# Performance work log

Measured on AMD Instinct MI355X. Metric: run time of the kernel, lower is better.

The kernel has to match this reference:

```python
import jax, jax.numpy as jnp
import numpy as np

D = 512       # d_model
H = 8         # n_heads per pathway MHA
CTX_H = 2     # router context_attention heads
P = 16        # num_attention_pathways
K = 8         # top_k_pathways
B = 8
S = 1024
TEMP = 1.0
RH1, RH2 = 128, 64  # router hidden sizes


def mha(x, in_w, in_b, out_w, out_b, n_heads):
    """torch.nn.MultiheadAttention (batch_first, eval mode, no mask)."""
    b, s, d = x.shape
    dh = d // n_heads
    qkv = x @ in_w.T + in_b                      # [b,s,3d]
    q, k, v = jnp.split(qkv, 3, axis=-1)
    sh = lambda t: t.reshape(b, s, n_heads, dh).transpose(0, 2, 1, 3)
    q, k, v = sh(q), sh(k), sh(v)
    scale = 1.0 / float(np.sqrt(dh))
    attn = jax.nn.softmax(jnp.einsum('bhqd,bhkd->bhqk', q, k) * scale, axis=-1)
    o = jnp.einsum('bhqk,bhkd->bhqd', attn, v).transpose(0, 2, 1, 3).reshape(b, s, d)
    return o @ out_w.T + out_b


def setup_inputs() -> dict:
    key = jax.random.key(0)
    ks = jax.random.split(key, 16)
    w = 0.05  # weight init scale to keep attention logits sane
    return {
        'x': jax.random.normal(ks[0], (B, S, D), jnp.float32),
        'ctx_in_w': jax.random.normal(ks[1], (3 * D, D), jnp.float32) * w,
        'ctx_in_b': jnp.zeros((3 * D,), jnp.float32),
        'ctx_out_w': jax.random.normal(ks[2], (D, D), jnp.float32) * w,
        'ctx_out_b': jnp.zeros((D,), jnp.float32),
        'r_w1': jax.random.normal(ks[3], (RH1, D), jnp.float32) * w,
        'r_b1': jnp.zeros((RH1,), jnp.float32),
        'r_w2': jax.random.normal(ks[4], (RH2, RH1), jnp.float32) * w,
        'r_b2': jnp.zeros((RH2,), jnp.float32),
        'r_w3': jax.random.normal(ks[5], (P, RH2), jnp.float32) * w,
        'r_b3': jnp.zeros((P,), jnp.float32),
        'p_in_w': jax.random.normal(ks[6], (P, 3 * D, D), jnp.float32) * w,
        'p_in_b': jnp.zeros((P, 3 * D), jnp.float32),
        'p_out_w': jax.random.normal(ks[7], (P, D, D), jnp.float32) * w,
        'p_out_b': jnp.zeros((P, D), jnp.float32),
    }


def reference(x, ctx_in_w, ctx_in_b, ctx_out_w, ctx_out_b,
              r_w1, r_b1, r_w2, r_b2, r_w3, r_b3,
              p_in_w, p_in_b, p_out_w, p_out_b):
    b, s, d = x.shape
    # --- SemanticPathwayRouter ---
    attended = mha(x, ctx_in_w, ctx_in_b, ctx_out_w, ctx_out_b, CTX_H)
    h = jax.nn.relu(attended @ r_w1.T + r_b1)
    h = jax.nn.relu(h @ r_w2.T + r_b2)
    pathway_scores = h @ r_w3.T + r_b3            # [b,s,P]
    # --- GLBL load-balance loss (eval: no buffer updates) ---
    probs_lb = jax.nn.softmax(pathway_scores, axis=-1)
    freq = probs_lb.mean(axis=(0, 1))             # [P] (frequencies == avg scores)
    glbl_loss = P * jnp.sum(freq * freq)
    # --- top-k gating: softmax -> topk scatter -> renormalize ---
    probs = jax.nn.softmax(pathway_scores / TEMP, axis=-1)
    top_v, top_i = jax.lax.top_k(probs, K)        # [b,s,K]
    bi = jnp.arange(b)[:, None, None]
    si = jnp.arange(s)[None, :, None]
    weights = jnp.zeros_like(probs).at[bi, si, top_i].set(top_v)
    weights = weights / (weights.sum(axis=-1, keepdims=True) + 1e-8)
    # --- combine: weighted sum of P full-MHA experts (scan keeps memory low) ---
    wp = jnp.moveaxis(weights, -1, 0)             # [P,b,s]
    def step(acc, params):
        iw, ib, ow, ob, wk = params
        return acc + mha(x, iw, ib, ow, ob, H) * wk[..., None], None
    output, _ = jax.lax.scan(step, jnp.zeros_like(x),
                             (p_in_w, p_in_b, p_out_w, p_out_b, wp))
    return output, glbl_loss, weights
```

## Files before the change

kernel.cpp:

```cpp
#include <hip/hip_runtime.h>
#include <math.h>

#define TOKENS 8192
#define DM 512
#define TD 1536
#define SEQ 1024
#define NPATH 16
#define TOPK 8

typedef __bf16 bf16x8v __attribute__((ext_vector_type(8)));
typedef __bf16 bf16x4v __attribute__((ext_vector_type(4)));
typedef float f32x4v __attribute__((ext_vector_type(4)));
typedef unsigned short u16x8 __attribute__((ext_vector_type(8)));

__device__ __forceinline__ void gload_lds16(const void* gp, unsigned lds_byte_off) {
    __builtin_amdgcn_global_load_lds(
        (const __attribute__((address_space(1))) unsigned int*)(uintptr_t)gp,
        (__attribute__((address_space(3))) unsigned int*)(uintptr_t)lds_byte_off,
        16, 0, 0);
}

__global__ __launch_bounds__(256)
void gemm_f32_nt(const float* __restrict__ A, const float* __restrict__ B,
                 const float* __restrict__ bias, float* __restrict__ C,
                 int M, int N, int K, int lda, int ldb, int ldc,
                 float alpha, int relu, int zmode)
{
    __shared__ float As[16][132];
    __shared__ float Bs[16][132];
    if (zmode == 1) {
        const int z = blockIdx.z, bb = z >> 1, hh = z & 1;
        A += (size_t)bb * SEQ * TD + hh * 256;
        B += (size_t)bb * SEQ * TD + 512 + hh * 256;
        C += (size_t)z * SEQ * SEQ;
    }
    const int tid = threadIdx.x;
    const int bm = blockIdx.y << 7, bn = blockIdx.x << 7;
    const int tx4 = (tid & 15) << 2, ty4 = ((tid >> 4) & 15) << 2;
    float acc[8][8] = {};
    for (int k0 = 0; k0 < K; k0 += 16) {
        __syncthreads();
#pragma unroll
        for (int it = 0; it < 2; ++it) {
            const int u = (it << 8) + tid;
            const int row = u >> 2, kc4 = (u & 3) << 2;
            const float4 av = *(const float4*)(A + (size_t)(bm + row) * lda + k0 + kc4);
            As[kc4 + 0][row] = av.x; As[kc4 + 1][row] = av.y;
            As[kc4 + 2][row] = av.z; As[kc4 + 3][row] = av.w;
            const float4 bv = *(const float4*)(B + (size_t)(bn + row) * ldb + k0 + kc4);
            Bs[kc4 + 0][row] = bv.x; Bs[kc4 + 1][row] = bv.y;
            Bs[kc4 + 2][row] = bv.z; Bs[kc4 + 3][row] = bv.w;
        }
        __syncthreads();
#pragma unroll
        for (int kk = 0; kk < 16; ++kk) {
            const float4 a0 = *(const float4*)&As[kk][ty4];
            const float4 a1 = *(const float4*)&As[kk][64 + ty4];
            const float4 b0 = *(const float4*)&Bs[kk][tx4];
            const float4 b1 = *(const float4*)&Bs[kk][64 + tx4];
            const float aa[8] = {a0.x, a0.y, a0.z, a0.w, a1.x, a1.y, a1.z, a1.w};
            const float bb[8] = {b0.x, b0.y, b0.z, b0.w, b1.x, b1.y, b1.z, b1.w};
#pragma unroll
            for (int i = 0; i < 8; ++i)
#pragma unroll
                for (int j = 0; j < 8; ++j)
                    acc[i][j] = fmaf(aa[i], bb[j], acc[i][j]);
        }
    }
    float bcol[8] = {};
    if (bias) {
        const float4 bL = *(const float4*)(bias + bn + tx4);
        const float4 bH = *(const float4*)(bias + bn + 64 + tx4);
        bcol[0] = bL.x; bcol[1] = bL.y; bcol[2] = bL.z; bcol[3] = bL.w;
        bcol[4] = bH.x; bcol[5] = bH.y; bcol[6] = bH.z; bcol[7] = bH.w;
    }
#pragma unroll
    for (int i = 0; i < 8; ++i) {
        const int row = bm + ((i < 4) ? (ty4 + i) : (64 + ty4 + i - 4));
        float* cp = C + (size_t)row * ldc + bn;
        float v[8];
#pragma unroll
        for (int j = 0; j < 8; ++j) {
            v[j] = alpha * acc[i][j] + bcol[j];
            if (relu) v[j] = fmaxf(v[j], 0.f);
        }
        *(float4*)(cp + tx4) = make_float4(v[0], v[1], v[2], v[3]);
        *(float4*)(cp + 64 + tx4) = make_float4(v[4], v[5], v[6], v[7]);
    }
}

__global__ __launch_bounds__(256)
void gemm_f32_pv(const float* __restrict__ Sb, const float* __restrict__ qkv,
                 float* __restrict__ obuf)
{
    __shared__ float As[16][132];
    __shared__ float Bs[16][128];
    const int z = blockIdx.z, bb = z >> 1, hh = z & 1;
    const float* A = Sb + (size_t)z * SEQ * SEQ;
    const float* B = qkv + (size_t)bb * SEQ * TD + 1024 + hh * 256;
    float* C = obuf + (size_t)bb * SEQ * 512 + hh * 256;
    const int tid = threadIdx.x;
    const int bm = blockIdx.y << 7, bn = blockIdx.x << 7;
    const int tx4 = (tid & 15) << 2, ty4 = ((tid >> 4) & 15) << 2;
    float acc[8][8] = {};
    for (int k0 = 0; k0 < SEQ; k0 += 16) {
        __syncthreads();
#pragma unroll
        for (int it = 0; it < 2; ++it) {
            const int u = (it << 8) + tid;
            const int row = u >> 2, kc4 = (u & 3) << 2;
            const float4 av = *(const float4*)(A + (size_t)(bm + row) * SEQ + k0 + kc4);
            As[kc4 + 0][row] = av.x; As[kc4 + 1][row] = av.y;
            As[kc4 + 2][row] = av.z; As[kc4 + 3][row] = av.w;
            const int krow = u >> 5, n4 = (u & 31) << 2;
            *(float4*)&Bs[krow][n4] = *(const float4*)(B + (size_t)(k0 + krow) * TD + bn + n4);
        }
        __syncthreads();
#pragma unroll
        for (int kk = 0; kk < 16; ++kk) {
            const float4 a0 = *(const float4*)&As[kk][ty4];
            const float4 a1 = *(const float4*)&As[kk][64 + ty4];
            const float4 b0 = *(const float4*)&Bs[kk][tx4];
            const float4 b1 = *(const float4*)&Bs[kk][64 + tx4];
            const float aa[8] = {a0.x, a0.y, a0.z, a0.w, a1.x, a1.y, a1.z, a1.w};
            const float bb[8] = {b0.x, b0.y, b0.z, b0.w, b1.x, b1.y, b1.z, b1.w};
#pragma unroll
            for (int i = 0; i < 8; ++i)
#pragma unroll
                for (int j = 0; j < 8; ++j)
                    acc[i][j] = fmaf(aa[i], bb[j], acc[i][j]);
        }
    }
#pragma unroll
    for (int i = 0; i < 8; ++i) {
        const int row = bm + ((i < 4) ? (ty4 + i) : (64 + ty4 + i - 4));
        float* cp = C + (size_t)row * 512 + bn;
        *(float4*)(cp + tx4) = make_float4(acc[i][0], acc[i][1], acc[i][2], acc[i][3]);
        *(float4*)(cp + 64 + tx4) = make_float4(acc[i][4], acc[i][5], acc[i][6], acc[i][7]);
    }
}

__global__ __launch_bounds__(256)
void softmax_rows(float* __restrict__ S_)
{
    const int row = blockIdx.x * 4 + (threadIdx.x >> 6);
    const int lane = threadIdx.x & 63;
    float* rp = S_ + (size_t)row * 1024 + lane * 16;
    float4 v[4];
#pragma unroll
    for (int i = 0; i < 4; ++i) v[i] = *(const float4*)(rp + i * 4);
    float mx = -INFINITY;
#pragma unroll
    for (int i = 0; i < 4; ++i)
        mx = fmaxf(mx, fmaxf(fmaxf(v[i].x, v[i].y), fmaxf(v[i].z, v[i].w)));
#pragma unroll
    for (int off = 1; off < 64; off <<= 1) mx = fmaxf(mx, __shfl_xor(mx, off));
    float sum = 0.f;
#pragma unroll
    for (int i = 0; i < 4; ++i) {
        v[i].x = __expf(v[i].x - mx); v[i].y = __expf(v[i].y - mx);
        v[i].z = __expf(v[i].z - mx); v[i].w = __expf(v[i].w - mx);
        sum += v[i].x + v[i].y + v[i].z + v[i].w;
    }
#pragma unroll
    for (int off = 1; off < 64; off <<= 1) sum += __shfl_xor(sum, off);
    const float inv = 1.f / sum;
#pragma unroll
    for (int i = 0; i < 4; ++i) {
        v[i].x *= inv; v[i].y *= inv; v[i].z *= inv; v[i].w *= inv;
        *(float4*)(rp + i * 4) = v[i];
    }
}

__global__ __launch_bounds__(256)
void gemm_f32(const float* __restrict__ A, const float* __restrict__ W,
              const float* __restrict__ bias, float* __restrict__ C,
              int M, int N, int K, int relu)
{
    __shared__ float As[16][64];
    __shared__ float Bs[16][64];
    const int bm = blockIdx.y << 6;
    const int bn = blockIdx.x << 6;
    const int tid = threadIdx.x;
    const int tx = tid & 15, ty = tid >> 4;
    const int lr = tid >> 2;
    const int lc = (tid & 3) << 2;
    float acc[4][4] = {};
    for (int k0 = 0; k0 < K; k0 += 16) {
        float4 av = *(const float4*)(A + (size_t)(bm + lr) * K + (k0 + lc));
        float4 bv = make_float4(0.f, 0.f, 0.f, 0.f);
        const int wr = bn + lr;
        if (wr < N) bv = *(const float4*)(W + (size_t)wr * K + (k0 + lc));
        __syncthreads();
        As[lc + 0][lr] = av.x; As[lc + 1][lr] = av.y;
        As[lc + 2][lr] = av.z; As[lc + 3][lr] = av.w;
        Bs[lc + 0][lr] = bv.x; Bs[lc + 1][lr] = bv.y;
        Bs[lc + 2][lr] = bv.z; Bs[lc + 3][lr] = bv.w;
        __syncthreads();
#pragma unroll
        for (int kk = 0; kk < 16; ++kk) {
            const float4 a4 = *(const float4*)(&As[kk][ty << 2]);
            const float4 b4 = *(const float4*)(&Bs[kk][tx << 2]);
            const float a[4] = {a4.x, a4.y, a4.z, a4.w};
            const float b[4] = {b4.x, b4.y, b4.z, b4.w};
#pragma unroll
            for (int i = 0; i < 4; ++i)
#pragma unroll
                for (int j = 0; j < 4; ++j)
                    acc[i][j] = fmaf(a[i], b[j], acc[i][j]);
        }
    }
#pragma unroll
    for (int i = 0; i < 4; ++i) {
        const int m = bm + (ty << 2) + i;
#pragma unroll
        for (int j = 0; j < 4; ++j) {
            const int n = bn + (tx << 2) + j;
            if (n < N) {
                float v = acc[i][j] + bias[n];
                if (relu) v = fmaxf(v, 0.f);
                C[(size_t)m * N + n] = v;
            }
        }
    }
}

template <int DH>
__global__ __launch_bounds__(256)
void flash_attn(const float* __restrict__ qkv, float* __restrict__ O,
                int H, float scale)
{
    constexpr int NU = DH / 64;
    __shared__ float Qs[32][DH + 4];
    __shared__ float Ks[32][DH + 4];
    __shared__ float Vs[32][DH + 4];
    __shared__ float Ps[32][33];
    const int tid = threadIdx.x;
    const int g2 = tid & 15;
    const int rs = tid >> 4;
    const int bh = blockIdx.y;
    const int b = bh / H, h = bh - b * H;
    const int rb = blockIdx.x << 5;
    const float* qb = qkv + (size_t)b * SEQ * TD + (size_t)h * DH;
    const float* kb = qb + DM;
    const float* vb = qb + 2 * DM;

    for (int idx = tid; idx < 32 * (DH / 4); idx += 256) {
        const int rr = idx / (DH / 4);
        const int dp = (idx - rr * (DH / 4)) << 2;
        float4 v = *(const float4*)(qb + (size_t)(rb + rr) * TD + dp);
        v.x *= scale; v.y *= scale; v.z *= scale; v.w *= scale;
        *(float4*)&Qs[rr][dp] = v;
    }
    float m0 = -INFINITY, m1 = -INFINITY, l0 = 0.f, l1 = 0.f;
    float4 o0[NU], o1[NU];
#pragma unroll
    for (int u = 0; u < NU; ++u) {
        o0[u] = make_float4(0.f, 0.f, 0.f, 0.f);
        o1[u] = make_float4(0.f, 0.f, 0.f, 0.f);
    }
    __syncthreads();

    for (int kt = 0; kt < SEQ; kt += 32) {
        for (int idx = tid; idx < 32 * (DH / 4); idx += 256) {
            const int rr = idx / (DH / 4);
            const int dp = (idx - rr * (DH / 4)) << 2;
            *(float4*)&Ks[rr][dp] = *(const float4*)(kb + (size_t)(kt + rr) * TD + dp);
            *(float4*)&Vs[rr][dp] = *(const float4*)(vb + (size_t)(kt + rr) * TD + dp);
        }
        __syncthreads();
        float s00 = 0.f, s01 = 0.f, s10 = 0.f, s11 = 0.f;
        const int cA = g2, cB = g2 + 16;
#pragma unroll 8
        for (int i = 0; i < DH; i += 4) {
            const float4 q0 = *(const float4*)&Qs[rs][i];
            const float4 q1 = *(const float4*)&Qs[rs + 16][i];
            const float4 k0 = *(const float4*)&Ks[cA][i];
            const float4 k1 = *(const float4*)&Ks[cB][i];
            s00 += q0.x * k0.x + q0.y * k0.y + q0.z * k0.z + q0.w * k0.w;
            s01 += q0.x * k1.x + q0.y * k1.y + q0.z * k1.z + q0.w * k1.w;
            s10 += q1.x * k0.x + q1.y * k0.y + q1.z * k0.z + q1.w * k0.w;
            s11 += q1.x * k1.x + q1.y * k1.y + q1.z * k1.z + q1.w * k1.w;
        }
        float ml0 = fmaxf(s00, s01), ml1 = fmaxf(s10, s11);
#pragma unroll
        for (int off = 1; off < 16; off <<= 1) {
            ml0 = fmaxf(ml0, __shfl_xor(ml0, off));
            ml1 = fmaxf(ml1, __shfl_xor(ml1, off));
        }
        const float n0 = fmaxf(m0, ml0), n1 = fmaxf(m1, ml1);
        const float f0 = __expf(m0 - n0), f1 = __expf(m1 - n1);
        const float p00 = __expf(s00 - n0), p01 = __expf(s01 - n0);
        const float p10 = __expf(s10 - n1), p11 = __expf(s11 - n1);
        float sum0 = p00 + p01, sum1 = p10 + p11;
#pragma unroll
        for (int off = 1; off < 16; off <<= 1) {
            sum0 += __shfl_xor(sum0, off);
            sum1 += __shfl_xor(sum1, off);
        }
        l0 = l0 * f0 + sum0; l1 = l1 * f1 + sum1;
        m0 = n0; m1 = n1;
#pragma unroll
        for (int u = 0; u < NU; ++u) {
            o0[u].x *= f0; o0[u].y *= f0; o0[u].z *= f0; o0[u].w *= f0;
            o1[u].x *= f1; o1[u].y *= f1; o1[u].z *= f1; o1[u].w *= f1;
        }
        Ps[rs][cA] = p00; Ps[rs][cB] = p01;
        Ps[rs + 16][cA] = p10; Ps[rs + 16][cB] = p11;
        __syncthreads();
#pragma unroll 4
        for (int c = 0; c < 32; ++c) {
            const float pv0 = Ps[rs][c];
            const float pv1 = Ps[rs + 16][c];
#pragma unroll
            for (int u = 0; u < NU; ++u) {
                const float4 v4 = *(const float4*)&Vs[c][(g2 << 2) + (u << 6)];
                o0[u].x = fmaf(pv0, v4.x, o0[u].x);
                o0[u].y = fmaf(pv0, v4.y, o0[u].y);
                o0[u].z = fmaf(pv0, v4.z, o0[u].z);
                o0[u].w = fmaf(pv0, v4.w, o0[u].w);
                o1[u].x = fmaf(pv1, v4.x, o1[u].x);
                o1[u].y = fmaf(pv1, v4.y, o1[u].y);
                o1[u].z = fmaf(pv1, v4.z, o1[u].z);
                o1[u].w = fmaf(pv1, v4.w, o1[u].w);
            }
        }
        __syncthreads();
    }
    const float i0 = 1.f / l0, i1 = 1.f / l1;
    float* ob0 = O + (size_t)b * SEQ * DM + (size_t)(rb + rs) * DM + h * DH;
    float* ob1 = ob0 + (size_t)16 * DM;
#pragma unroll
    for (int u = 0; u < NU; ++u) {
        float4 w0 = o0[u];
        w0.x *= i0; w0.y *= i0; w0.z *= i0; w0.w *= i0;
        *(float4*)(ob0 + (g2 << 2) + (u << 6)) = w0;
        float4 w1 = o1[u];
        w1.x *= i1; w1.y *= i1; w1.z *= i1; w1.w *= i1;
        *(float4*)(ob1 + (g2 << 2) + (u << 6)) = w1;
    }
}

__global__ __launch_bounds__(256)
void router_epilogue(const float* __restrict__ scores, float* __restrict__ freq,
                     float* __restrict__ weights)
{
    const int t = blockIdx.x * 256 + threadIdx.x;
    float s[NPATH];
#pragma unroll
    for (int i = 0; i < NPATH; ++i) s[i] = scores[(size_t)t * NPATH + i];
    float mx = s[0];
#pragma unroll
    for (int i = 1; i < NPATH; ++i) mx = fmaxf(mx, s[i]);
    float p[NPATH];
    float sum = 0.f;
#pragma unroll
    for (int i = 0; i < NPATH; ++i) { p[i] = expf(s[i] - mx); sum += p[i]; }
    const float inv = 1.f / sum;
#pragma unroll
    for (int i = 0; i < NPATH; ++i) p[i] *= inv;
#pragma unroll
    for (int i = 0; i < NPATH; ++i) {
        float v = p[i];
        for (int off = 32; off >= 1; off >>= 1) v += __shfl_xor(v, off);
        if ((threadIdx.x & 63) == 0) atomicAdd(&freq[i], v);
    }
    unsigned used = 0u;
    float topv[TOPK];
    int topi[TOPK];
    float wsum = 0.f;
#pragma unroll
    for (int k = 0; k < TOPK; ++k) {
        float best = -1.f; int bi = 0;
#pragma unroll
        for (int i = 0; i < NPATH; ++i) {
            if (!((used >> i) & 1u) && p[i] > best) { best = p[i]; bi = i; }
        }
        used |= 1u << bi;
        topv[k] = best; topi[k] = bi;
        wsum += best;
    }
    const float winv = 1.f / (wsum + 1e-8f);
    float w[NPATH];
#pragma unroll
    for (int i = 0; i < NPATH; ++i) w[i] = 0.f;
#pragma unroll
    for (int k = 0; k < TOPK; ++k) w[topi[k]] = topv[k] * winv;
#pragma unroll
    for (int i = 0; i < NPATH; ++i) weights[(size_t)t * NPATH + i] = w[i];
}

__global__ void glbl_loss_kernel(const float* __restrict__ freq, float* __restrict__ out)
{
    if (threadIdx.x == 0 && blockIdx.x == 0) {
        float acc = 0.f;
        for (int i = 0; i < NPATH; ++i) {
            const float f = freq[i] * (1.f / (float)TOKENS);
            acc += f * f;
        }
        out[0] = (float)NPATH * acc;
    }
}

__global__ __launch_bounds__(256)
void cast_f32_bf16(const float* __restrict__ src, __bf16* __restrict__ dst, int n)
{
    const int i = (blockIdx.x * 256 + threadIdx.x) * 4;
    if (i < n) {
        const float4 v = *(const float4*)(src + i);
        bf16x4v o;
        o[0] = (__bf16)v.x; o[1] = (__bf16)v.y; o[2] = (__bf16)v.z; o[3] = (__bf16)v.w;
        *(bf16x4v*)(dst + i) = o;
    }
}

__global__ __launch_bounds__(256)
void gemm_bf16_qkv(const __bf16* __restrict__ A, const __bf16* __restrict__ B,
                   const float* __restrict__ bias, __bf16* __restrict__ C,
                   int N, int K)
{
    __shared__ __attribute__((aligned(16))) __bf16 As[128 * 32];
    __shared__ __attribute__((aligned(16))) __bf16 Bs[128 * 32];
    const int tid = threadIdx.x;
    const int l = tid & 63, w = tid >> 6;
    const int wr = w >> 1, wc = w & 1;
    const int a16 = l & 15, g = l >> 4;
    const int bm = blockIdx.y << 7, bn = blockIdx.x << 7;
    const unsigned asA = (unsigned)(uintptr_t)(void*)&As[0];
    const unsigned asB = (unsigned)(uintptr_t)(void*)&Bs[0];

    f32x4v acc[4][4] = {};
    for (int k0 = 0; k0 < K; k0 += 32) {
        __syncthreads();
#pragma unroll
        for (int it = 0; it < 2; ++it) {
            const int u = it * 256 + tid;
            const int row = u >> 2, cc = u & 3;
            const unsigned dst = (unsigned)((it * 256 + w * 64) * 16);
            gload_lds16(A + (size_t)(bm + row) * K + k0 + cc * 8, asA + dst);
            gload_lds16(B + (size_t)(bn + row) * K + k0 + cc * 8, asB + dst);
        }
        __syncthreads();
        bf16x8v af[4], bf[4];
#pragma unroll
        for (int m = 0; m < 4; ++m)
            af[m] = *(const bf16x8v*)&As[(wr * 64 + m * 16 + a16) * 32 + g * 8];
#pragma unroll
        for (int n = 0; n < 4; ++n)
            bf[n] = *(const bf16x8v*)&Bs[(wc * 64 + n * 16 + a16) * 32 + g * 8];
#pragma unroll
        for (int m = 0; m < 4; ++m)
#pragma unroll
            for (int n = 0; n < 4; ++n)
                acc[m][n] = __builtin_amdgcn_mfma_f32_16x16x32_bf16(af[m], bf[n], acc[m][n], 0, 0, 0);
    }
#pragma unroll
    for (int n = 0; n < 4; ++n) {
        const int col = bn + wc * 64 + n * 16 + a16;
        const float bv = bias[col];
        const float sc = (col < DM) ? 0.125f : 1.0f;
#pragma unroll
        for (int m = 0; m < 4; ++m) {
            const int row0 = bm + wr * 64 + m * 16 + g * 4;
#pragma unroll
            for (int r = 0; r < 4; ++r)
                C[(size_t)(row0 + r) * N + col] = (__bf16)((acc[m][n][r] + bv) * sc);
        }
    }
}

__global__ __launch_bounds__(256)
void gemm_bf16_out(const __bf16* __restrict__ A, const __bf16* __restrict__ B,
                   const float* __restrict__ bias, const float* __restrict__ wts,
                   float* __restrict__ out, int path, int first)
{
    __shared__ __attribute__((aligned(16))) __bf16 As[128 * 32];
    __shared__ __attribute__((aligned(16))) __bf16 Bs[128 * 32];
    const int tid = threadIdx.x;
    const int l = tid & 63, w = tid >> 6;
    const int wr = w >> 1, wc = w & 1;
    const int a16 = l & 15, g = l >> 4;
    const int bm = blockIdx.y << 7, bn = blockIdx.x << 7;
    const unsigned asA = (unsigned)(uintptr_t)(void*)&As[0];
    const unsigned asB = (unsigned)(uintptr_t)(void*)&Bs[0];

    f32x4v acc[4][4] = {};
    for (int k0 = 0; k0 < DM; k0 += 32) {
        __syncthreads();
#pragma unroll
        for (int it = 0; it < 2; ++it) {
            const int u = it * 256 + tid;
            const int row = u >> 2, cc = u & 3;
            const unsigned dst = (unsigned)((it * 256 + w * 64) * 16);
            gload_lds16(A + (size_t)(bm + row) * DM + k0 + cc * 8, asA + dst);
            gload_lds16(B + (size_t)(bn + row) * DM + k0 + cc * 8, asB + dst);
        }
        __syncthreads();
        bf16x8v af[4], bf[4];
#pragma unroll
        for (int m = 0; m < 4; ++m)
            af[m] = *(const bf16x8v*)&As[(wr * 64 + m * 16 + a16) * 32 + g * 8];
#pragma unroll
        for (int n = 0; n < 4; ++n)
            bf[n] = *(const bf16x8v*)&Bs[(wc * 64 + n * 16 + a16) * 32 + g * 8];
#pragma unroll
        for (int m = 0; m < 4; ++m)
#pragma unroll
            for (int n = 0; n < 4; ++n)
                acc[m][n] = __builtin_amdgcn_mfma_f32_16x16x32_bf16(af[m], bf[n], acc[m][n], 0, 0, 0);
    }
#pragma unroll
    for (int m = 0; m < 4; ++m) {
        const int row0 = bm + wr * 64 + m * 16 + g * 4;
#pragma unroll
        for (int r = 0; r < 4; ++r) {
            const int row = row0 + r;
            const float wk = wts[(size_t)row * NPATH + path];
#pragma unroll
            for (int n = 0; n < 4; ++n) {
                const int col = bn + wc * 64 + n * 16 + a16;
                const float v = (acc[m][n][r] + bias[col]) * wk;
                const size_t oi = (size_t)row * DM + col;
                if (first) out[oi] = v; else out[oi] += v;
            }
        }
    }
}

__global__ __launch_bounds__(256)
void attn_bf16(const __bf16* __restrict__ qkv, __bf16* __restrict__ O)
{
    __shared__ __attribute__((aligned(16))) __bf16 Ks[64 * 72];
    __shared__ __attribute__((aligned(16))) __bf16 Vt[64 * 72];
    __shared__ __attribute__((aligned(16))) __bf16 Pq[4][32 * 72];
    const int tid = threadIdx.x;
    const int l = tid & 63, w = tid >> 6;
    const int a = l & 15, g = l >> 4;
    const int bh = blockIdx.y;
    const int b = bh >> 3, h = bh & 7;
    const int qb = blockIdx.x << 7;
    const size_t base = (size_t)b * SEQ * TD;

    bf16x8v qA0, qA1, qB0, qB1;
    {
        const __bf16* qp = qkv + base + (size_t)(qb + w * 32 + a) * TD + h * 64 + g * 8;
        qA0 = *(const bf16x8v*)qp;
        qA1 = *(const bf16x8v*)(qp + 32);
        const __bf16* qp2 = qp + (size_t)16 * TD;
        qB0 = *(const bf16x8v*)qp2;
        qB1 = *(const bf16x8v*)(qp2 + 32);
    }
    float lA = 0.f, lB = 0.f;
    f32x4v oA[4] = {}, oB[4] = {};
    __bf16* pw = &Pq[w][0];
    const int sc8 = tid & 7;
    const int sr  = tid >> 3;
    const int vcol8 = (sr >> 2) ^ sc8;

    bf16x8v kpre0, kpre1, vpre0, vpre1;
    {
        const __bf16* kp0 = qkv + base + (size_t)sr * TD + DM + h * 64 + sc8 * 8;
        kpre0 = *(const bf16x8v*)kp0;
        kpre1 = *(const bf16x8v*)(kp0 + (size_t)32 * TD);
        const __bf16* vp0 = qkv + base + (size_t)(2 * sr) * TD + 2 * DM + h * 64 + sc8 * 8;
        vpre0 = *(const bf16x8v*)vp0;
        vpre1 = *(const bf16x8v*)(vp0 + TD);
    }

    for (int kt = 0; kt < SEQ; kt += 64) {
        __syncthreads();

        *(bf16x8v*)&Ks[sr * 72 + sc8 * 8] = kpre0;
        *(bf16x8v*)&Ks[(32 + sr) * 72 + sc8 * 8] = kpre1;
        {
            const u16x8 v0 = __builtin_bit_cast(u16x8, vpre0);
            const u16x8 v1 = __builtin_bit_cast(u16x8, vpre1);
#pragma unroll
            for (int j = 0; j < 8; ++j) {
                const unsigned pk = (unsigned)v0[j] | ((unsigned)v1[j] << 16);
                *(unsigned*)&Vt[(sc8 * 8 + j) * 72 + vcol8 * 8 + (sr & 3) * 2] = pk;
            }
        }
        if (kt + 64 < SEQ) {
            const __bf16* kp0 = qkv + base + (size_t)(kt + 64 + sr) * TD + DM + h * 64 + sc8 * 8;
            kpre0 = *(const bf16x8v*)kp0;
            kpre1 = *(const bf16x8v*)(kp0 + (size_t)32 * TD);
            const __bf16* vp0 = qkv + base + (size_t)(kt + 64 + 2 * sr) * TD + 2 * DM + h * 64 + sc8 * 8;
            vpre0 = *(const bf16x8v*)vp0;
            vpre1 = *(const bf16x8v*)(vp0 + TD);
        }
        __syncthreads();

        f32x4v sA[4] = {}, sB[4] = {};
        __builtin_amdgcn_s_setprio(1);
#pragma unroll
        for (int kc = 0; kc < 4; ++kc) {
            const bf16x8v kf0 = *(const bf16x8v*)&Ks[(kc * 16 + a) * 72 + g * 8];
            const bf16x8v kf1 = *(const bf16x8v*)&Ks[(kc * 16 + a) * 72 + 32 + g * 8];
            sA[kc] = __builtin_amdgcn_mfma_f32_16x16x32_bf16(kf0, qA0, sA[kc], 0, 0, 0);
            sA[kc] = __builtin_amdgcn_mfma_f32_16x16x32_bf16(kf1, qA1, sA[kc], 0, 0, 0);
            sB[kc] = __builtin_amdgcn_mfma_f32_16x16x32_bf16(kf0, qB0, sB[kc], 0, 0, 0);
            sB[kc] = __builtin_amdgcn_mfma_f32_16x16x32_bf16(kf1, qB1, sB[kc], 0, 0, 0);
        }
        __builtin_amdgcn_s_setprio(0);

        float lsumA = 0.f, lsumB = 0.f;
#pragma unroll
        for (int kc = 0; kc < 4; ++kc) {
            bf16x4v pkA, pkB;
#pragma unroll
            for (int r = 0; r < 4; ++r) {
                const float pA = __expf(sA[kc][r]);
                const float pB = __expf(sB[kc][r]);
                lsumA += pA; lsumB += pB;
                pkA[r] = (__bf16)pA; pkB[r] = (__bf16)pB;
            }
            *(bf16x4v*)&pw[a * 72 + kc * 16 + g * 4] = pkA;
            *(bf16x4v*)&pw[(16 + a) * 72 + kc * 16 + g * 4] = pkB;
        }
        lsumA += __shfl_xor(lsumA, 16);
        lsumA += __shfl_xor(lsumA, 32);
        lsumB += __shfl_xor(lsumB, 16);
        lsumB += __shfl_xor(lsumB, 32);
        lA += lsumA; lB += lsumB;
        asm volatile("s_waitcnt lgkmcnt(0)" ::: "memory");

        __builtin_amdgcn_s_setprio(1);
#pragma unroll
        for (int dc = 0; dc < 4; ++dc) {
            const int vrow = dc * 16 + a;
#pragma unroll
            for (int kh = 0; kh < 2; ++kh) {
                const bf16x8v vf = *(const bf16x8v*)&Vt[vrow * 72 + ((((kh << 2) + g) ^ ((vrow >> 3) & 7)) & 7) * 8];
                const bf16x8v paA = *(const bf16x8v*)&pw[a * 72 + kh * 32 + g * 8];
                const bf16x8v paB = *(const bf16x8v*)&pw[(16 + a) * 72 + kh * 32 + g * 8];
                oA[dc] = __builtin_amdgcn_mfma_f32_16x16x32_bf16(paA, vf, oA[dc], 0, 0, 0);
                oB[dc] = __builtin_amdgcn_mfma_f32_16x16x32_bf16(paB, vf, oB[dc], 0, 0, 0);
            }
        }
        __builtin_amdgcn_s_setprio(0);
    }

    float liA[4], liB[4];
#pragma unroll
    for (int r = 0; r < 4; ++r) {
        liA[r] = 1.f / __shfl(lA, 4 * g + r);
        liB[r] = 1.f / __shfl(lB, 4 * g + r);
    }
    const int row0 = qb + w * 32 + g * 4;
#pragma unroll
    for (int dc = 0; dc < 4; ++dc)
#pragma unroll
        for (int r = 0; r < 4; ++r) {
            O[(size_t)(b * SEQ + row0 + r) * DM + h * 64 + dc * 16 + a] = (__bf16)(oA[dc][r] * liA[r]);
            O[(size_t)(b * SEQ + row0 + 16 + r) * DM + h * 64 + dc * 16 + a] = (__bf16)(oB[dc][r] * liB[r]);
        }
}

extern "C" void kernel_launch(void* const* d_in, const int* in_sizes, int n_in,
                              void* d_out, int out_size, void* d_ws, size_t ws_size,
                              hipStream_t stream)
{
    const float* x         = (const float*)d_in[0];
    const float* ctx_in_w  = (const float*)d_in[1];
    const float* ctx_in_b  = (const float*)d_in[2];
    const float* ctx_out_w = (const float*)d_in[3];
    const float* ctx_out_b = (const float*)d_in[4];
    const float* r_w1      = (const float*)d_in[5];
    const float* r_b1      = (const float*)d_in[6];
    const float* r_w2      = (const float*)d_in[7];
    const float* r_b2      = (const float*)d_in[8];
    const float* r_w3      = (const float*)d_in[9];
    const float* r_b3      = (const float*)d_in[10];
    const float* p_in_w    = (const float*)d_in[11];
    const float* p_in_b    = (const float*)d_in[12];
    const float* p_out_w   = (const float*)d_in[13];
    const float* p_out_b   = (const float*)d_in[14];

    float* out  = (float*)d_out;
    float* loss = out + (size_t)TOKENS * DM;
    float* wts  = loss + 1;

    float* F = (float*)d_ws;
    float* qkvbuf   = F;
    float* obuf     = F + 12582912;
    float* attended = F;
    float* h1       = F + 4194304;
    float* h2       = F + 5242880;
    float* scores   = F + 5767168;
    float* freq     = F + 5898240;

    const int M = TOKENS;
    dim3 blk(256);
    const bool big = ws_size >= (size_t)134217728;

    hipMemsetAsync(freq, 0, NPATH * sizeof(float), stream);
    gemm_f32_nt<<<dim3(TD / 128, M / 128), blk, 0, stream>>>(
        x, ctx_in_w, ctx_in_b, qkvbuf, M, TD, DM, DM, DM, TD, 1.f, 0, 0);
    if (big) {
        float* Sbuf = F + 16777216;
        gemm_f32_nt<<<dim3(8, 8, 16), blk, 0, stream>>>(
            qkvbuf, qkvbuf, nullptr, Sbuf, SEQ, SEQ, 256, TD, TD, SEQ, 0.0625f, 0, 1);
        softmax_rows<<<dim3(16 * SEQ / 4), blk, 0, stream>>>(Sbuf);
        gemm_f32_pv<<<dim3(2, 8, 16), blk, 0, stream>>>(Sbuf, qkvbuf, obuf);
    } else {
        flash_attn<256><<<dim3(SEQ / 32, 8 * 2), blk, 0, stream>>>(qkvbuf, obuf, 2, 1.f / 16.f);
    }
    gemm_f32_nt<<<dim3(DM / 128, M / 128), blk, 0, stream>>>(
        obuf, ctx_out_w, ctx_out_b, attended, M, DM, DM, DM, DM, DM, 1.f, 0, 0);
    gemm_f32_nt<<<dim3(1, M / 128), blk, 0, stream>>>(
        attended, r_w1, r_b1, h1, M, 128, DM, DM, DM, 128, 1.f, 1, 0);
    gemm_f32<<<dim3(1, M / 64), blk, 0, stream>>>(h1, r_w2, r_b2, h2, M, 64, 128, 1);
    gemm_f32<<<dim3(1, M / 64), blk, 0, stream>>>(h2, r_w3, r_b3, scores, M, NPATH, 64, 0);
    router_epilogue<<<dim3(TOKENS / 256), blk, 0, stream>>>(scores, freq, wts);
    glbl_loss_kernel<<<dim3(1), dim3(64), 0, stream>>>(freq, loss);

    if (big) {
        __bf16* xb       = (__bf16*)F;
        __bf16* qkv_b    = (__bf16*)(F + 2097152);
        __bf16* obuf_b   = (__bf16*)(F + 8388608);
        __bf16* wqkv_all = (__bf16*)(F + 16777216);
        __bf16* wout_all = (__bf16*)(F + 23068672);
        cast_f32_bf16<<<dim3(TOKENS * DM / 4 / 256), blk, 0, stream>>>(x, xb, TOKENS * DM);
        cast_f32_bf16<<<dim3(NPATH * TD * DM / 4 / 256), blk, 0, stream>>>(
            p_in_w, wqkv_all, NPATH * TD * DM);
        cast_f32_bf16<<<dim3(NPATH * DM * DM / 4 / 256), blk, 0, stream>>>(
            p_out_w, wout_all, NPATH * DM * DM);
        for (int p = 0; p < NPATH; ++p) {
            gemm_bf16_qkv<<<dim3(TD / 128, M / 128), blk, 0, stream>>>(
                xb, wqkv_all + (size_t)p * TD * DM, p_in_b + (size_t)p * TD, qkv_b, TD, DM);
            attn_bf16<<<dim3(SEQ / 128, 64), blk, 0, stream>>>(qkv_b, obuf_b);
            gemm_bf16_out<<<dim3(DM / 128, M / 128), blk, 0, stream>>>(
                obuf_b, wout_all + (size_t)p * DM * DM, p_out_b + (size_t)p * DM, wts, out, p, p == 0);
        }
    } else {
        __bf16* xb     = (__bf16*)F;
        __bf16* qkv_b  = (__bf16*)(F + 2097152);
        __bf16* obuf_b = (__bf16*)(F + 8388608);
        __bf16* wqkv_b = (__bf16*)(F + 12582912);
        __bf16* wout_b = (__bf16*)(F + 12976128);
        cast_f32_bf16<<<dim3(TOKENS * DM / 4 / 256), blk, 0, stream>>>(x, xb, TOKENS * DM);
        for (int p = 0; p < NPATH; ++p) {
            cast_f32_bf16<<<dim3(TD * DM / 4 / 256), blk, 0, stream>>>(
                p_in_w + (size_t)p * TD * DM, wqkv_b, TD * DM);
            cast_f32_bf16<<<dim3(DM * DM / 4 / 256), blk, 0, stream>>>(
                p_out_w + (size_t)p * DM * DM, wout_b, DM * DM);
            gemm_bf16_qkv<<<dim3(TD / 128, M / 128), blk, 0, stream>>>(
                xb, wqkv_b, p_in_b + (size_t)p * TD, qkv_b, TD, DM);
            attn_bf16<<<dim3(SEQ / 128, 64), blk, 0, stream>>>(qkv_b, obuf_b);
            gemm_bf16_out<<<dim3(DM / 128, M / 128), blk, 0, stream>>>(
                obuf_b, wout_b, p_out_b + (size_t)p * DM, wts, out, p, p == 0);
        }
    }
}
```

Measured before the change: 2.132 ms.

## Split pathway attention across two KV halves with a combine kernel

Replaces the per-pathway attention kernel with a split-K variant that processes each half of the key/value sequence in a separate block. Partial fp32 outputs and row sums go to workspace, and a new combine kernel adds them and normalises into bf16. The goal is to double the attention grid from 512 to 1024 blocks for better occupancy of the GPU's compute units. The cost is an extra kernel launch per pathway plus fp32 partial-output traffic of about 32 MB written and read per pathway. The softmax has no max subtraction, so adding the halves directly is exact, which matches the existing kernel's approach.

```diff
diff --git a/kernel.cpp b/kernel.cpp
--- a/kernel.cpp
+++ b/kernel.cpp
@@ -569,7 +569,6 @@
 
     for (int kt = 0; kt < SEQ; kt += 64) {
         __syncthreads();
-
         *(bf16x8v*)&Ks[sr * 72 + sc8 * 8] = kpre0;
         *(bf16x8v*)&Ks[(32 + sr) * 72 + sc8 * 8] = kpre1;
         {
@@ -655,6 +654,160 @@
             O[(size_t)(b * SEQ + row0 + r) * DM + h * 64 + dc * 16 + a] = (__bf16)(oA[dc][r] * liA[r]);
             O[(size_t)(b * SEQ + row0 + 16 + r) * DM + h * 64 + dc * 16 + a] = (__bf16)(oB[dc][r] * liB[r]);
         }
+}
+
+__global__ __launch_bounds__(256)
+void attn_bf16_splitk(const __bf16* __restrict__ qkv, float* __restrict__ Opart,
+                      float* __restrict__ lpart)
+{
+    __shared__ __attribute__((aligned(16))) __bf16 Ks[64 * 72];
+    __shared__ __attribute__((aligned(16))) __bf16 Vt[64 * 72];
+    __shared__ __attribute__((aligned(16))) __bf16 Pq[4][32 * 72];
+    const int tid = threadIdx.x;
+    const int l = tid & 63, w = tid >> 6;
+    const int a = l & 15, g = l >> 4;
+    const int bh = blockIdx.y;
+    const int b = bh >> 3, h = bh & 7;
+    const int qb = blockIdx.x << 7;
+    const int z = blockIdx.z;
+    const int kv0 = z << 9;
+    const size_t base = (size_t)b * SEQ * TD;
+
+    bf16x8v qA0, qA1, qB0, qB1;
+    {
+        const __bf16* qp = qkv + base + (size_t)(qb + w * 32 + a) * TD + h * 64 + g * 8;
+        qA0 = *(const bf16x8v*)qp;
+        qA1 = *(const bf16x8v*)(qp + 32);
+        const __bf16* qp2 = qp + (size_t)16 * TD;
+        qB0 = *(const bf16x8v*)qp2;
+        qB1 = *(const bf16x8v*)(qp2 + 32);
+    }
+    float lA = 0.f, lB = 0.f;
+    f32x4v oA[4] = {}, oB[4] = {};
+    __bf16* pw = &Pq[w][0];
+    const int sc8 = tid & 7;
+    const int sr  = tid >> 3;
+    const int vcol8 = (sr >> 2) ^ sc8;
+
+    bf16x8v kpre0, kpre1, vpre0, vpre1;
+    {
+        const __bf16* kp0 = qkv + base + (size_t)(kv0 + sr) * TD + DM + h * 64 + sc8 * 8;
+        kpre0 = *(const bf16x8v*)kp0;
+        kpre1 = *(const bf16x8v*)(kp0 + (size_t)32 * TD);
+        const __bf16* vp0 = qkv + base + (size_t)(kv0 + 2 * sr) * TD + 2 * DM + h * 64 + sc8 * 8;
+        vpre0 = *(const bf16x8v*)vp0;
+        vpre1 = *(const bf16x8v*)(vp0 + TD);
+    }
+
+    for (int kt = kv0; kt < kv0 + 512; kt += 64) {
+        __syncthreads();
+        *(bf16x8v*)&Ks[sr * 72 + sc8 * 8] = kpre0;
+        *(bf16x8v*)&Ks[(32 + sr) * 72 + sc8 * 8] = kpre1;
+        {
+            const u16x8 v0 = __builtin_bit_cast(u16x8, vpre0);
+            const u16x8 v1 = __builtin_bit_cast(u16x8, vpre1);
+#pragma unroll
+            for (int j = 0; j < 8; ++j) {
+                const unsigned pk = (unsigned)v0[j] | ((unsigned)v1[j] << 16);
+                *(unsigned*)&Vt[(sc8 * 8 + j) * 72 + vcol8 * 8 + (sr & 3) * 2] = pk;
+            }
+        }
+        if (kt + 64 < kv0 + 512) {
+            const __bf16* kp0 = qkv + base + (size_t)(kt + 64 + sr) * TD + DM + h * 64 + sc8 * 8;
+            kpre0 = *(const bf16x8v*)kp0;
+            kpre1 = *(const bf16x8v*)(kp0 + (size_t)32 * TD);
+            const __bf16* vp0 = qkv + base + (size_t)(kt + 64 + 2 * sr) * TD + 2 * DM + h * 64 + sc8 * 8;
+            vpre0 = *(const bf16x8v*)vp0;
+            vpre1 = *(const bf16x8v*)(vp0 + TD);
+        }
+        __syncthreads();
+
+        f32x4v sA[4] = {}, sB[4] = {};
+        __builtin_amdgcn_s_setprio(1);
+#pragma unroll
+        for (int kc = 0; kc < 4; ++kc) {
+            const bf16x8v kf0 = *(const bf16x8v*)&Ks[(kc * 16 + a) * 72 + g * 8];
+            const bf16x8v kf1 = *(const bf16x8v*)&Ks[(kc * 16 + a) * 72 + 32 + g * 8];
+            sA[kc] = __builtin_amdgcn_mfma_f32_16x16x32_bf16(kf0, qA0, sA[kc], 0, 0, 0);
+            sA[kc] = __builtin_amdgcn_mfma_f32_16x16x32_bf16(kf1, qA1, sA[kc], 0, 0, 0);
+            sB[kc] = __builtin_amdgcn_mfma_f32_16x16x32_bf16(kf0, qB0, sB[kc], 0, 0, 0);
+            sB[kc] = __builtin_amdgcn_mfma_f32_16x16x32_bf16(kf1, qB1, sB[kc], 0, 0, 0);
+        }
+        __builtin_amdgcn_s_setprio(0);
+
+        float lsumA = 0.f, lsumB = 0.f;
+#pragma unroll
+        for (int kc = 0; kc < 4; ++kc) {
+            bf16x4v pkA, pkB;
+#pragma unroll
+            for (int r = 0; r < 4; ++r) {
+                const float pA = __expf(sA[kc][r]);
+                const float pB = __expf(sB[kc][r]);
+                lsumA += pA; lsumB += pB;
+                pkA[r] = (__bf16)pA; pkB[r] = (__bf16)pB;
+            }
+            *(bf16x4v*)&pw[a * 72 + kc * 16 + g * 4] = pkA;
+            *(bf16x4v*)&pw[(16 + a) * 72 + kc * 16 + g * 4] = pkB;
+        }
+        lsumA += __shfl_xor(lsumA, 16);
+        lsumA += __shfl_xor(lsumA, 32);
+        lsumB += __shfl_xor(lsumB, 16);
+        lsumB += __shfl_xor(lsumB, 32);
+        lA += lsumA; lB += lsumB;
+        asm volatile("s_waitcnt lgkmcnt(0)" ::: "memory");
+
+        __builtin_amdgcn_s_setprio(1);
+#pragma unroll
+        for (int dc = 0; dc < 4; ++dc) {
+            const int vrow = dc * 16 + a;
+#pragma unroll
+            for (int kh = 0; kh < 2; ++kh) {
+                const bf16x8v vf = *(const bf16x8v*)&Vt[vrow * 72 + ((((kh << 2) + g) ^ ((vrow >> 3) & 7)) & 7) * 8];
+                const bf16x8v paA = *(const bf16x8v*)&pw[a * 72 + kh * 32 + g * 8];
+                const bf16x8v paB = *(const bf16x8v*)&pw[(16 + a) * 72 + kh * 32 + g * 8];
+                oA[dc] = __builtin_amdgcn_mfma_f32_16x16x32_bf16(paA, vf, oA[dc], 0, 0, 0);
+                oB[dc] = __builtin_amdgcn_mfma_f32_16x16x32_bf16(paB, vf, oB[dc], 0, 0, 0);
+            }
+        }
+        __builtin_amdgcn_s_setprio(0);
+    }
+
+    float* opz = Opart + (size_t)z * TOKENS * DM;
+    const int row0 = qb + w * 32 + g * 4;
+#pragma unroll
+    for (int dc = 0; dc < 4; ++dc)
+#pragma unroll
+        for (int r = 0; r < 4; ++r) {
+            opz[(size_t)(b * SEQ + row0 + r) * DM + h * 64 + dc * 16 + a] = oA[dc][r];
+            opz[(size_t)(b * SEQ + row0 + 16 + r) * DM + h * 64 + dc * 16 + a] = oB[dc][r];
+        }
+    if (g == 0) {
+        lpart[(size_t)z * 65536 + bh * 1024 + qb + w * 32 + a] = lA;
+        lpart[(size_t)z * 65536 + bh * 1024 + qb + w * 32 + 16 + a] = lB;
+    }
+}
+
+__global__ __launch_bounds__(256)
+void attn_combine(const float* __restrict__ Opart, const float* __restrict__ lpart,
+                  __bf16* __restrict__ O)
+{
+    const int i = (blockIdx.x * 256 + threadIdx.x) * 4;
+    const int tok = i >> 9;
+    const int col = i & 511;
+    const int b = tok >> 10, srow = tok & 1023;
+    const int h = col >> 6;
+    const int bh = b * 8 + h;
+    const float l0 = lpart[bh * 1024 + srow];
+    const float l1 = lpart[65536 + bh * 1024 + srow];
+    const float inv = 1.f / (l0 + l1);
+    const float4 o0 = *(const float4*)(Opart + i);
+    const float4 o1 = *(const float4*)(Opart + 4194304 + i);
+    bf16x4v r;
+    r[0] = (__bf16)((o0.x + o1.x) * inv);
+    r[1] = (__bf16)((o0.y + o1.y) * inv);
+    r[2] = (__bf16)((o0.z + o1.z) * inv);
+    r[3] = (__bf16)((o0.w + o1.w) * inv);
+    *(bf16x4v*)(O + i) = r;
 }
 
 extern "C" void kernel_launch(void* const* d_in, const int* in_sizes, int n_in,
@@ -719,8 +872,10 @@
         __bf16* xb       = (__bf16*)F;
         __bf16* qkv_b    = (__bf16*)(F + 2097152);
         __bf16* obuf_b   = (__bf16*)(F + 8388608);
+        float*  lpart    = F + 10485760;
         __bf16* wqkv_all = (__bf16*)(F + 16777216);
         __bf16* wout_all = (__bf16*)(F + 23068672);
+        float*  Opart    = F + 25165824;
         cast_f32_bf16<<<dim3(TOKENS * DM / 4 / 256), blk, 0, stream>>>(x, xb, TOKENS * DM);
         cast_f32_bf16<<<dim3(NPATH * TD * DM / 4 / 256), blk, 0, stream>>>(
             p_in_w, wqkv_all, NPATH * TD * DM);
@@ -729,7 +884,8 @@
         for (int p = 0; p < NPATH; ++p) {
             gemm_bf16_qkv<<<dim3(TD / 128, M / 128), blk, 0, stream>>>(
                 xb, wqkv_all + (size_t)p * TD * DM, p_in_b + (size_t)p * TD, qkv_b, TD, DM);
-            attn_bf16<<<dim3(SEQ / 128, 64), blk, 0, stream>>>(qkv_b, obuf_b);
+            attn_bf16_splitk<<<dim3(SEQ / 128, 64, 2), blk, 0, stream>>>(qkv_b, Opart, lpart);
+            attn_combine<<<dim3(TOKENS * DM / 4 / 256), blk, 0, stream>>>(Opart, lpart, obuf_b);
             gemm_bf16_out<<<dim3(DM / 128, M / 128), blk, 0, stream>>>(
                 obuf_b, wout_all + (size_t)p * DM * DM, p_out_b + (size_t)p * DM, wts, out, p, p == 0);
         }
```

Measured after the change: 2.275 ms. 1.07x slower.
